# Kernel optimization log

Measured on AMD Instinct MI355X. Metric: run time of the kernel, lower is better.

Reference implementation:

```python
import jax, jax.numpy as jnp
import numpy as np

NA, NW, H = 20000, 100000, 128
DA, DW = 64, 128
E_CR, E_IN, E_CO = 400000, 600000, 300000


def _seg_softmax(logits, seg, n):
    m = jax.ops.segment_max(logits, seg, num_segments=n)
    e = jnp.exp(logits - m[seg])
    s = jax.ops.segment_sum(e, seg, num_segments=n)
    return e / (s[seg] + 1e-16)


def _gat(x_src, x_dst, edge, W, b, a_s, a_d):
    # PyG GATConv, heads=1, concat=False, shared lin for src/dst, add_self_loops=True
    n_src, n_dst = x_src.shape[0], x_dst.shape[0]
    loops = jnp.arange(min(n_src, n_dst), dtype=edge.dtype)
    src = jnp.concatenate([edge[0], loops])
    dst = jnp.concatenate([edge[1], loops])
    hs = x_src @ W            # [n_src, H]
    hd = x_dst @ W            # [n_dst, H]
    logit = jax.nn.leaky_relu((hs @ a_s)[src] + (hd @ a_d)[dst], 0.2)
    alpha = _seg_softmax(logit, dst, n_dst)          # softmax over in-neighborhoods
    out = jax.ops.segment_sum(alpha[:, None] * hs[src], dst, num_segments=n_dst)
    return out + b


def _mlp2(x, w1, b1, w2, b2):
    return jax.nn.relu(x @ w1 + b1) @ w2 + b2


def setup_inputs() -> dict:
    key = jax.random.key(0)
    ks = iter(jax.random.split(key, 40))

    def p(shape, scale=0.1):
        return jax.random.normal(next(ks), shape, jnp.float32) * scale

    def edges(n_src, n_dst, E):
        s = jax.random.randint(next(ks), (E,), 0, n_src, dtype=jnp.int32)
        d = jax.random.randint(next(ks), (E,), 0, n_dst, dtype=jnp.int32)
        d = jnp.where(s == d, (d + 1) % n_dst, d)  # keep input loop-free (PyG strips them)
        return jnp.stack([s, d])

    e_creates = edges(NA, NW, E_CR)
    inp = {
        'artist_feat': jax.random.normal(next(ks), (NA, DA), jnp.float32),
        'work_feat': jax.random.normal(next(ks), (NW, DW), jnp.float32),
        'a_w1': p((DA, H)), 'a_b1': jnp.zeros(H, jnp.float32),
        'a_w2': p((H, H)), 'a_b2': jnp.zeros(H, jnp.float32),
        'w_w1': p((DW, H)), 'w_b1': jnp.zeros(H, jnp.float32),
        'w_w2': p((H, H)), 'w_b2': jnp.zeros(H, jnp.float32),
        'cr_W': p((H, H)), 'cr_b': jnp.zeros(H, jnp.float32), 'cr_as': p((H,)), 'cr_ad': p((H,)),
        'in_W': p((H, H)), 'in_b': jnp.zeros(H, jnp.float32), 'in_as': p((H,)), 'in_ad': p((H,)),
        'co_W': p((H, H)), 'co_b': jnp.zeros(H, jnp.float32), 'co_as': p((H,)), 'co_ad': p((H,)),
        'p_w1': p((2 * H, 256)), 'p_b1': jnp.zeros(256, jnp.float32),
        'p_w2': p((256, 128)), 'p_b2': jnp.zeros(128, jnp.float32),
        'p_w3': p((128, 1)), 'p_b3': jnp.zeros(1, jnp.float32),
        'e_creates': e_creates,
        'e_created_by': jnp.flip(e_creates, axis=0),  # reverse relation [work, artist]
        'e_infl': edges(NW, NW, E_IN),
        'e_collab': edges(NA, NA, E_CO),
    }
    return inp


def reference(artist_feat, work_feat,
              a_w1, a_b1, a_w2, a_b2,
              w_w1, w_b1, w_w2, w_b2,
              cr_W, cr_b, cr_as, cr_ad,
              in_W, in_b, in_as, in_ad,
              co_W, co_b, co_as, co_ad,
              p_w1, p_b1, p_w2, p_b2, p_w3, p_b3,
              e_creates, e_created_by, e_infl, e_collab):
    ax = _mlp2(artist_feat, a_w1, a_b1, a_w2, a_b2)      # [NA, H]
    wx = _mlp2(work_feat, w_w1, w_b1, w_w2, w_b2)        # [NW, H]
    wx = jax.nn.elu(_gat(ax, wx, e_creates, cr_W, cr_b, cr_as, cr_ad))
    wx = jax.nn.elu(_gat(wx, wx, e_infl, in_W, in_b, in_as, in_ad))
    au = _gat(wx, ax, e_created_by, cr_W, cr_b, cr_as, cr_ad)  # no elu (matches source)
    ac = jax.nn.elu(_gat(au, au, e_collab, co_W, co_b, co_as, co_ad))
    comb = jnp.concatenate([au, ac], axis=1)             # [NA, 2H]
    h = jax.nn.relu(comb @ p_w1 + p_b1)                  # dropout is identity in eval
    h = jax.nn.relu(h @ p_w2 + p_b2)
    return (h @ p_w3 + p_b3).squeeze()
```

## Files before the change

### kernel.cpp

```cpp
#include <hip/hip_runtime.h>
#include <hip/hip_bf16.h>
#include <cstddef>

#define NA 20000
#define NW 100000
#define HH 128
#define DA 64
#define E_CR 400000
#define E_IN 600000
#define E_CO 300000

#define ROW1 0
#define ROW2 (NW)
#define ROW3 (2 * NW)
#define ROW4 (2 * NW + NA)
#define NTOT (2 * NW + 2 * NA)
#define CAPW 40
#define CAPA 88
#define NPREP (10 * 128 + 1)
#define GNB ((NA + 127) / 128)

typedef short v8s __attribute__((ext_vector_type(8)));
typedef float v4f __attribute__((ext_vector_type(4)));

constexpr int PSLOT = 2 * 128 * 264;

__device__ inline short f2bf(float x) {
    union { float f; unsigned u; } c; c.f = x;
    unsigned r = c.u + 0x7fff + ((c.u >> 16) & 1);
    return (short)(r >> 16);
}
__device__ inline float bf2f(short s) {
    union { unsigned u; float f; } c; c.u = ((unsigned)(unsigned short)s) << 16;
    return c.f;
}
__device__ inline float bfu2f(unsigned short s) {
    union { unsigned u; float f; } c; c.u = ((unsigned)s) << 16;
    return c.f;
}

__device__ inline void split8(const float* xv, v8s& h, v8s& l) {
#pragma unroll
    for (int p = 0; p < 4; ++p) {
        float2 xf; xf.x = xv[2 * p]; xf.y = xv[2 * p + 1];
        __hip_bfloat162 hb = __float22bfloat162_rn(xf);
        float2 hf = __bfloat1622float2(hb);
        float2 lf; lf.x = xf.x - hf.x; lf.y = xf.y - hf.y;
        __hip_bfloat162 lb = __float22bfloat162_rn(lf);
        union { __hip_bfloat162 b; short2 s; } uh, ul;
        uh.b = hb; ul.b = lb;
        h[2 * p] = uh.s.x; h[2 * p + 1] = uh.s.y;
        l[2 * p] = ul.s.x; l[2 * p + 1] = ul.s.y;
    }
}

struct AppChunk { const int* e; int E; int* pad; int cap; int* deg; };

__device__ inline void do_append(const AppChunk& ap, int bid) {
    int b0 = bid * 1024 + threadIdx.x;
    int s[4], d[4]; bool ok[4];
#pragma unroll
    for (int u = 0; u < 4; ++u) {
        int i = b0 + u * 256;
        ok[u] = i < ap.E;
        s[u] = 0; d[u] = 0;
        if (ok[u]) { s[u] = ap.e[i]; d[u] = ap.e[ap.E + i]; }
    }
    int p[4];
#pragma unroll
    for (int u = 0; u < 4; ++u) if (ok[u]) p[u] = atomicAdd(&ap.deg[d[u]], 1);
#pragma unroll
    for (int u = 0; u < 4; ++u)
        if (ok[u] && p[u] < ap.cap)
            ap.pad[(size_t)d[u] * ap.cap + p[u]] = s[u];
}

struct PrepDesc { const float* src; int ldw; int K; };
struct PrepArgs {
    PrepDesc d[10]; const float* wvW; const float* wvA; float* vd;
    const float* gX; const float* gB; float* gY; int gM;
};

__global__ __launch_bounds__(256) void k_prep_append(PrepArgs a, short* __restrict__ out,
                                                    AppChunk ap)
{
    __shared__ short Bs2[2 * 128 * 72];
    if (blockIdx.x >= NPREP + GNB) { do_append(ap, blockIdx.x - NPREP - GNB); return; }
    if (blockIdx.x >= NPREP) {
        int bid = blockIdx.x - NPREP;
        const int tid = threadIdx.x;
        const int wave = tid >> 6, lane = tid & 63;
        const int l15 = lane & 15, quad = lane >> 4;
        const int wrow = bid * 128 + wave * 32;
        for (int e = tid; e < 64 * 128; e += 256) {
            int n = e & 127, k = e >> 7;
            float x = a.d[0].src[(size_t)k * 128 + n];
            short h = f2bf(x);
            short l = f2bf(x - bf2f(h));
            Bs2[n * 72 + k] = h;
            Bs2[128 * 72 + n * 72 + k] = l;
        }
        v8s ah[2][2], al[2][2];
#pragma unroll
        for (int rf = 0; rf < 2; ++rf) {
            int r = wrow + rf * 16 + l15; if (r >= a.gM) r = a.gM - 1;
            const float* xp = a.gX + (size_t)r * DA + quad * 8;
#pragma unroll
            for (int kf = 0; kf < 2; ++kf) {
                float xv[8];
                *(float4*)&xv[0] = *(const float4*)(xp + kf * 32);
                *(float4*)&xv[4] = *(const float4*)(xp + kf * 32 + 4);
                split8(xv, ah[rf][kf], al[rf][kf]);
            }
        }
        __syncthreads();
        v4f acc[2][8];
#pragma unroll
        for (int rf = 0; rf < 2; ++rf)
#pragma unroll
            for (int cf = 0; cf < 8; ++cf) acc[rf][cf] = (v4f){0.f, 0.f, 0.f, 0.f};
#pragma unroll
        for (int kf = 0; kf < 2; ++kf) {
#pragma unroll
            for (int cf = 0; cf < 8; ++cf) {
                int coff = (cf * 16 + l15) * 72 + kf * 32 + quad * 8;
                v8s bh = *(const v8s*)&Bs2[coff];
                v8s bl = *(const v8s*)&Bs2[128 * 72 + coff];
#pragma unroll
                for (int rf = 0; rf < 2; ++rf) {
                    acc[rf][cf] = __builtin_amdgcn_mfma_f32_16x16x32_bf16(al[rf][kf], bh, acc[rf][cf], 0, 0, 0);
                    acc[rf][cf] = __builtin_amdgcn_mfma_f32_16x16x32_bf16(ah[rf][kf], bl, acc[rf][cf], 0, 0, 0);
                    acc[rf][cf] = __builtin_amdgcn_mfma_f32_16x16x32_bf16(ah[rf][kf], bh, acc[rf][cf], 0, 0, 0);
                }
            }
        }
        float bv[8];
#pragma unroll
        for (int cf = 0; cf < 8; ++cf) bv[cf] = a.gB[cf * 16 + l15];
#pragma unroll
        for (int rf = 0; rf < 2; ++rf) {
#pragma unroll
            for (int reg = 0; reg < 4; ++reg) {
                int r = wrow + rf * 16 + quad * 4 + reg;
                if (r >= a.gM) continue;
                float* yp = a.gY + (size_t)r * HH;
#pragma unroll
                for (int cf = 0; cf < 8; ++cf) {
                    float o = acc[rf][cf][reg] + bv[cf];
                    yp[cf * 16 + l15] = o > 0.f ? o : 0.f;
                }
            }
        }
        return;
    }
    if (blockIdx.x == NPREP - 1) {
        __shared__ float sa[HH];
        int t = threadIdx.x;
        if (t < HH) sa[t] = a.wvA[t];
        __syncthreads();
        if (t < HH) {
            float s = 0.f;
            for (int jj = 0; jj < HH; ++jj) s += a.wvW[(size_t)t * HH + jj] * sa[jj];
            a.vd[t] = s;
        }
        return;
    }
    int m = blockIdx.x >> 7;
    int e = (blockIdx.x & 127) * 256 + threadIdx.x;
    PrepDesc dd = a.d[m];
    int K = dd.K;
    int KP = (K <= 128) ? K + 8 : K;
    if (e >= K * 128) return;
    int n = e & 127, k = e >> 7;
    float x = dd.src[(size_t)k * dd.ldw + n];
    short h = f2bf(x);
    short l = f2bf(x - bf2f(h));
    short* base = out + (size_t)m * PSLOT;
    base[n * KP + k] = h;
    base[128 * KP + n * KP + k] = l;
}

template<int K, int ACT, int NSS, int ST, int LDSB, int OBF, int DUAL, int XBF>
__global__ __launch_bounds__(256, 2) void k_mfma(
    const float* __restrict__ X, int ldx,
    const short* __restrict__ Wp,
    const float* __restrict__ bias,
    float* __restrict__ Y, int ldy, int M,
    const float* __restrict__ v1, float* __restrict__ ss1,
    const float* __restrict__ v2, float* __restrict__ ss2,
    const float* __restrict__ sb)
{
    constexpr int KF = K / 32;
    constexpr int KP = LDSB ? K + 8 : K;
    __shared__ short Bs[LDSB ? 2 * 128 * (K + 8) : 8];
    const int tid = threadIdx.x;
    const int wave = tid >> 6, lane = tid & 63;
    const int l15 = lane & 15, quad = lane >> 4;
    int bid = blockIdx.x;
    if (DUAL) {
        int g0 = gridDim.x >> 1;
        if (bid >= g0) { bid -= g0; Wp += PSLOT; bias += 128; Y += 128; }
    }
    const int wrow = bid * 128 + wave * 32;

    if (LDSB) {
        const float4* src = (const float4*)Wp;
        float4* dst = (float4*)Bs;
        constexpr int total = 2 * 128 * KP / 8;
        for (int i = tid; i < total; i += 256) dst[i] = src[i];
    }

    v4f acc[2][8];
#pragma unroll
    for (int rf = 0; rf < 2; ++rf)
#pragma unroll
        for (int cf = 0; cf < 8; ++cf) acc[rf][cf] = (v4f){0.f, 0.f, 0.f, 0.f};

    v8s ah[2][KF], al[2][KF];
#pragma unroll
    for (int rf = 0; rf < 2; ++rf) {
        int r = wrow + rf * 16 + l15; if (r >= M) r = M - 1;
        if (XBF) {
            const unsigned short* xp = (const unsigned short*)X + (size_t)r * ldx + quad * 8;
#pragma unroll
            for (int kf = 0; kf < KF; ++kf)
                ah[rf][kf] = *(const v8s*)(xp + kf * 32);
        } else {
            const float* xp = X + (size_t)r * ldx + quad * 8;
#pragma unroll
            for (int kf = 0; kf < KF; ++kf) {
                float xv[8];
                *(float4*)&xv[0] = *(const float4*)(xp + kf * 32);
                *(float4*)&xv[4] = *(const float4*)(xp + kf * 32 + 4);
                split8(xv, ah[rf][kf], al[rf][kf]);
            }
        }
    }
    if (LDSB) __syncthreads();
#pragma unroll
    for (int kf = 0; kf < KF; ++kf) {
#pragma unroll
        for (int cf = 0; cf < 8; ++cf) {
            const short* bp = LDSB ? &Bs[(cf * 16 + l15) * KP + kf * 32 + quad * 8]
                                   : Wp + (size_t)(cf * 16 + l15) * K + kf * 32 + quad * 8;
            v8s bh = *(const v8s*)bp;
            v8s bl = *(const v8s*)(bp + 128 * KP);
#pragma unroll
            for (int rf = 0; rf < 2; ++rf) {
                if (!XBF) acc[rf][cf] = __builtin_amdgcn_mfma_f32_16x16x32_bf16(al[rf][kf], bh, acc[rf][cf], 0, 0, 0);
                acc[rf][cf] = __builtin_amdgcn_mfma_f32_16x16x32_bf16(ah[rf][kf], bl, acc[rf][cf], 0, 0, 0);
                acc[rf][cf] = __builtin_amdgcn_mfma_f32_16x16x32_bf16(ah[rf][kf], bh, acc[rf][cf], 0, 0, 0);
            }
        }
    }

    float bv[8], v1c[8], v2c[8];
#pragma unroll
    for (int cf = 0; cf < 8; ++cf) {
        int col = cf * 16 + l15;
        bv[cf] = bias ? bias[col] : 0.f;
        if (NSS >= 1) v1c[cf] = v1[col];
        if (NSS >= 2) v2c[cf] = v2[col];
    }
    float sbv = (NSS >= 1 && sb) ? sb[0] : 0.f;

#pragma unroll
    for (int rf = 0; rf < 2; ++rf) {
#pragma unroll
        for (int reg = 0; reg < 4; ++reg) {
            int r = wrow + rf * 16 + quad * 4 + reg;
            if (r >= M) continue;
            float p1 = 0.f, p2 = 0.f;
#pragma unroll
            for (int cf = 0; cf < 8; ++cf) {
                float o = acc[rf][cf][reg] + bv[cf];
                if (ACT == 1) o = o > 0.f ? o : 0.f;
                if (NSS >= 1) p1 = fmaf(o, v1c[cf], p1);
                if (NSS >= 2) p2 = fmaf(o, v2c[cf], p2);
                if (ST) {
                    if (OBF) ((unsigned short*)Y)[(size_t)r * ldy + cf * 16 + l15] = (unsigned short)f2bf(o);
                    else     Y[(size_t)r * ldy + cf * 16 + l15] = o;
                }
            }
            if (NSS >= 1) {
#pragma unroll
                for (int w = 1; w < 16; w <<= 1) {
                    p1 += __shfl_xor(p1, w, 64);
                    if (NSS >= 2) p2 += __shfl_xor(p2, w, 64);
                }
                if (l15 == 0) {
                    ss1[r] = p1 + sbv;
                    if (NSS >= 2) ss2[r] = p2;
                }
            }
        }
    }
}

struct MfmaCfg {
    const float* X; int ldx;
    const short* Wp;
    const float* bias;
    float* Y; int ldy; int M;
    int act, nss, obf, xbf, st;
    const float* v1; float* ss1;
    const float* v2; float* ss2;
    int nblocks;
};

__global__ __launch_bounds__(256, 2) void k_mfma2(MfmaCfg c0, MfmaCfg c1, AppChunk ap)
{
    constexpr int KF = 4, KP = 136;
    __shared__ short Bs[2 * 128 * KP];
    int bid = blockIdx.x;
    if (bid >= c0.nblocks + c1.nblocks) { do_append(ap, bid - c0.nblocks - c1.nblocks); return; }
    const bool first = bid < c0.nblocks;
    const MfmaCfg& c = first ? c0 : c1;
    if (!first) bid -= c0.nblocks;
    const int tid = threadIdx.x;
    const int wave = tid >> 6, lane = tid & 63;
    const int l15 = lane & 15, quad = lane >> 4;
    const int wrow = bid * 128 + wave * 32;

    {
        const float4* src = (const float4*)c.Wp;
        float4* dst = (float4*)Bs;
        constexpr int total = 2 * 128 * KP / 8;
        for (int i = tid; i < total; i += 256) dst[i] = src[i];
    }

    v4f acc[2][8];
#pragma unroll
    for (int rf = 0; rf < 2; ++rf)
#pragma unroll
        for (int cf = 0; cf < 8; ++cf) acc[rf][cf] = (v4f){0.f, 0.f, 0.f, 0.f};

    v8s ah[2][KF], al[2][KF];
#pragma unroll
    for (int rf = 0; rf < 2; ++rf) {
        int r = wrow + rf * 16 + l15; if (r >= c.M) r = c.M - 1;
        if (c.xbf) {
            const unsigned short* xp = (const unsigned short*)c.X + (size_t)r * c.ldx + quad * 8;
#pragma unroll
            for (int kf = 0; kf < KF; ++kf) {
                ah[rf][kf] = *(const v8s*)(xp + kf * 32);
                al[rf][kf] = (v8s)(short)0;
            }
        } else {
            const float* xp = c.X + (size_t)r * c.ldx + quad * 8;
#pragma unroll
            for (int kf = 0; kf < KF; ++kf) {
                float xv[8];
                *(float4*)&xv[0] = *(const float4*)(xp + kf * 32);
                *(float4*)&xv[4] = *(const float4*)(xp + kf * 32 + 4);
                split8(xv, ah[rf][kf], al[rf][kf]);
            }
        }
    }
    __syncthreads();
#pragma unroll
    for (int kf = 0; kf < KF; ++kf) {
#pragma unroll
        for (int cf = 0; cf < 8; ++cf) {
            const short* bp = &Bs[(cf * 16 + l15) * KP + kf * 32 + quad * 8];
            v8s bh = *(const v8s*)bp;
            v8s bl = *(const v8s*)(bp + 128 * KP);
#pragma unroll
            for (int rf = 0; rf < 2; ++rf) {
                if (!c.xbf) acc[rf][cf] = __builtin_amdgcn_mfma_f32_16x16x32_bf16(al[rf][kf], bh, acc[rf][cf], 0, 0, 0);
                acc[rf][cf] = __builtin_amdgcn_mfma_f32_16x16x32_bf16(ah[rf][kf], bl, acc[rf][cf], 0, 0, 0);
                acc[rf][cf] = __builtin_amdgcn_mfma_f32_16x16x32_bf16(ah[rf][kf], bh, acc[rf][cf], 0, 0, 0);
            }
        }
    }

    float bv[8], v1c[8], v2c[8];
#pragma unroll
    for (int cf = 0; cf < 8; ++cf) {
        int col = cf * 16 + l15;
        bv[cf] = c.bias ? c.bias[col] : 0.f;
        v1c[cf] = (c.nss >= 1) ? c.v1[col] : 0.f;
        v2c[cf] = (c.nss >= 2) ? c.v2[col] : 0.f;
    }

#pragma unroll
    for (int rf = 0; rf < 2; ++rf) {
#pragma unroll
        for (int reg = 0; reg < 4; ++reg) {
            int r = wrow + rf * 16 + quad * 4 + reg;
            if (r >= c.M) continue;
            float p1 = 0.f, p2 = 0.f;
#pragma unroll
            for (int cf = 0; cf < 8; ++cf) {
                float o = acc[rf][cf][reg] + bv[cf];
                if (c.act) o = o > 0.f ? o : 0.f;
                p1 = fmaf(o, v1c[cf], p1);
                p2 = fmaf(o, v2c[cf], p2);
                if (c.st) {
                    if (c.obf) ((unsigned short*)c.Y)[(size_t)r * c.ldy + cf * 16 + l15] = (unsigned short)f2bf(o);
                    else       c.Y[(size_t)r * c.ldy + cf * 16 + l15] = o;
                }
            }
            if (c.nss >= 1) {
#pragma unroll
                for (int w = 1; w < 16; w <<= 1) {
                    p1 += __shfl_xor(p1, w, 64);
                    p2 += __shfl_xor(p2, w, 64);
                }
                if (l15 == 0) {
                    c.ss1[r] = p1;
                    if (c.nss >= 2) c.ss2[r] = p2;
                }
            }
        }
    }
}

template<int ELU, int U, int CAP, int OBF>
__global__ __launch_bounds__(256) void k_aggregate(
    const int* __restrict__ deg, const int* __restrict__ esp,
    const unsigned short* __restrict__ hs, const float* __restrict__ ss,
    const float* __restrict__ sd, const float* __restrict__ bias,
    void* __restrict__ out, int ldy, int n, int loopn)
{
    int lane = threadIdx.x & 63;
    int wv = threadIdx.x >> 6;
    int d = blockIdx.x * 4 + wv;
    if (d >= n) return;
    int half = lane >> 5;
    int col = (lane & 31) * 4;
    const int* row = esp + (size_t)d * CAP;
    int i1 = deg[d]; if (i1 > CAP) i1 = CAP;
    float sdv = sd[d];
    float den = 0.f;
    float ax = 0.f, ay = 0.f, az = 0.f, aw = 0.f;
    if (half == 0 && d < loopn) {
        ushort4 h = *(const ushort4*)(hs + (size_t)d * HH + col);
        float l = ss[d] + sdv;
        l = l < 0.f ? 0.2f * l : l;
        float e = __expf(l);
        den += e;
        ax = fmaf(e, bfu2f(h.x), ax);
        ay = fmaf(e, bfu2f(h.y), ay);
        az = fmaf(e, bfu2f(h.z), az);
        aw = fmaf(e, bfu2f(h.w), aw);
    }
    int i = 0;
    for (; i + 2 * U <= i1; i += 2 * U) {
        int s[U]; ushort4 h[U]; float sv[U];
#pragma unroll
        for (int u = 0; u < U; ++u) s[u] = row[i + 2 * u + half];
#pragma unroll
        for (int u = 0; u < U; ++u) h[u] = *(const ushort4*)(hs + (size_t)s[u] * HH + col);
#pragma unroll
        for (int u = 0; u < U; ++u) sv[u] = ss[s[u]];
#pragma unroll
        for (int u = 0; u < U; ++u) {
            float l = sv[u] + sdv;
            l = l < 0.f ? 0.2f * l : l;
            float e = __expf(l);
            den += e;
            ax = fmaf(e, bfu2f(h[u].x), ax);
            ay = fmaf(e, bfu2f(h[u].y), ay);
            az = fmaf(e, bfu2f(h[u].z), az);
            aw = fmaf(e, bfu2f(h[u].w), aw);
        }
    }
    if (i < i1) {
        int s[U]; ushort4 h[U]; float sv[U]; bool act[U];
#pragma unroll
        for (int u = 0; u < U; ++u) {
            int idx = i + 2 * u + half;
            act[u] = idx < i1;
            s[u] = row[act[u] ? idx : (i1 - 1)];
        }
#pragma unroll
        for (int u = 0; u < U; ++u) h[u] = *(const ushort4*)(hs + (size_t)s[u] * HH + col);
#pragma unroll
        for (int u = 0; u < U; ++u) sv[u] = ss[s[u]];
#pragma unroll
        for (int u = 0; u < U; ++u) {
            float l = sv[u] + sdv;
            l = l < 0.f ? 0.2f * l : l;
            float e = act[u] ? __expf(l) : 0.f;
            den += e;
            ax = fmaf(e, bfu2f(h[u].x), ax);
            ay = fmaf(e, bfu2f(h[u].y), ay);
            az = fmaf(e, bfu2f(h[u].z), az);
            aw = fmaf(e, bfu2f(h[u].w), aw);
        }
    }
    den += __shfl_xor(den, 32, 64);
    ax += __shfl_xor(ax, 32, 64);
    ay += __shfl_xor(ay, 32, 64);
    az += __shfl_xor(az, 32, 64);
    aw += __shfl_xor(aw, 32, 64);
    if (half == 0) {
        float4 b = *(const float4*)(bias + col);
        float inv = 1.f / (den + 1e-16f);
        float o0 = ax * inv + b.x;
        float o1 = ay * inv + b.y;
        float o2 = az * inv + b.z;
        float o3 = aw * inv + b.w;
        if (ELU) {
            o0 = o0 > 0.f ? o0 : expm1f(o0);
            o1 = o1 > 0.f ? o1 : expm1f(o1);
            o2 = o2 > 0.f ? o2 : expm1f(o2);
            o3 = o3 > 0.f ? o3 : expm1f(o3);
        }
        if (OBF) {
            ushort4 ob;
            ob.x = (unsigned short)f2bf(o0);
            ob.y = (unsigned short)f2bf(o1);
            ob.z = (unsigned short)f2bf(o2);
            ob.w = (unsigned short)f2bf(o3);
            *(ushort4*)((unsigned short*)out + (size_t)d * ldy + col) = ob;
        } else {
            *(float4*)((float*)out + (size_t)d * ldy + col) = make_float4(o0, o1, o2, o3);
        }
    }
}

extern "C" void kernel_launch(void* const* d_in, const int* in_sizes, int n_in,
                              void* d_out, int out_size, void* d_ws, size_t ws_size,
                              hipStream_t stream)
{
    const float* artist = (const float*)d_in[0];
    const float* workf  = (const float*)d_in[1];
    const float* a_w1 = (const float*)d_in[2];  const float* a_b1 = (const float*)d_in[3];
    const float* a_w2 = (const float*)d_in[4];  const float* a_b2 = (const float*)d_in[5];
    const float* w_w1 = (const float*)d_in[6];  const float* w_b1 = (const float*)d_in[7];
    const float* w_w2 = (const float*)d_in[8];  const float* w_b2 = (const float*)d_in[9];
    const float* cr_W = (const float*)d_in[10]; const float* cr_b = (const float*)d_in[11];
    const float* cr_as = (const float*)d_in[12]; const float* cr_ad = (const float*)d_in[13];
    const float* in_W = (const float*)d_in[14]; const float* in_b = (const float*)d_in[15];
    const float* in_as = (const float*)d_in[16]; const float* in_ad = (const float*)d_in[17];
    const float* co_W = (const float*)d_in[18]; const float* co_b = (const float*)d_in[19];
    const float* co_as = (const float*)d_in[20]; const float* co_ad = (const float*)d_in[21];
    const float* p_w1 = (const float*)d_in[22]; const float* p_b1 = (const float*)d_in[23];
    const float* p_w2 = (const float*)d_in[24]; const float* p_b2 = (const float*)d_in[25];
    const float* p_w3 = (const float*)d_in[26]; const float* p_b3 = (const float*)d_in[27];
    const int* e_cr = (const int*)d_in[28];
    const int* e_cb = (const int*)d_in[29];
    const int* e_in = (const int*)d_in[30];
    const int* e_co = (const int*)d_in[31];

    char* wsp = (char*)d_ws;
    size_t off = 0;
    auto alloc = [&](size_t bytes) -> void* {
        void* p = wsp + off;
        off += (bytes + 255) / 256 * 256;
        return p;
    };
    float* ax   = (float*)alloc((size_t)NA * HH * 4);
    float* hsA  = (float*)alloc((size_t)NA * HH * 4);
    unsigned short* hsw = (unsigned short*)alloc((size_t)NW * HH * 2);
    unsigned short* wxb = (unsigned short*)alloc((size_t)NW * HH * 2);
    unsigned short* hsb = (unsigned short*)alloc((size_t)NW * HH * 2);
    float* h1   = (float*)alloc((size_t)NA * 256 * 4);
    float* comb = (float*)alloc((size_t)NA * 256 * 4);
    float* ss1 = (float*)alloc((size_t)NA * 4);
    float* sd1 = (float*)alloc((size_t)NW * 4);
    float* ss2 = (float*)alloc((size_t)NW * 4);
    float* sd2 = (float*)alloc((size_t)NW * 4);
    float* ss3 = (float*)alloc((size_t)NW * 4);
    float* sd3 = (float*)alloc((size_t)NA * 4);
    float* ss4 = (float*)alloc((size_t)NA * 4);
    float* sd4 = (float*)alloc((size_t)NA * 4);
    float* vd  = (float*)alloc(HH * 4);
    int* deg   = (int*)alloc((size_t)NTOT * 4);
    int* pad1  = (int*)alloc((size_t)NW * CAPW * 4);
    int* pad2  = (int*)alloc((size_t)NW * CAPW * 4);
    int* pad3  = (int*)alloc((size_t)NA * CAPA * 4);
    int* pad4  = (int*)alloc((size_t)NA * CAPA * 4);
    short* preW = (short*)alloc((size_t)10 * PSLOT * 2);
    (void)ws_size; (void)in_sizes; (void)n_in; (void)out_size;

    auto pre = [&](int m) { return preW + (size_t)m * PSLOT; };
    auto gg = [](int M) { return (M + 127) / 128; };
    auto apb = [](int E) { return (E + 1023) / 1024; };
    const float* nf = nullptr;
    float* nfm = nullptr;

    PrepArgs pa;
    pa.d[0] = {a_w1, HH, DA};
    pa.d[1] = {a_w2, HH, HH};
    pa.d[2] = {w_w1, HH, HH};
    pa.d[3] = {w_w2, HH, HH};
    pa.d[4] = {cr_W, HH, HH};
    pa.d[5] = {in_W, HH, HH};
    pa.d[6] = {co_W, HH, HH};
    pa.d[7] = {p_w1, 256, 256};
    pa.d[8] = {p_w1 + 128, 256, 256};
    pa.d[9] = {p_w2, HH, 256};
    pa.wvW = cr_W; pa.wvA = cr_ad; pa.vd = vd;
    pa.gX = artist; pa.gB = a_b1; pa.gY = hsA; pa.gM = NA;

    AppChunk ap1 = {e_cr, E_CR, pad1, CAPW, deg + ROW1};
    AppChunk ap2 = {e_in, E_IN, pad2, CAPW, deg + ROW2};
    AppChunk ap3 = {e_cb, E_CR, pad3, CAPA, deg + ROW3};
    AppChunk ap4 = {e_co, E_CO, pad4, CAPA, deg + ROW4};

    (void)hipMemsetAsync(deg, 0, (size_t)NTOT * 4, stream);

    k_prep_append<<<NPREP + GNB + apb(E_CR), 256, 0, stream>>>(pa, preW, ap1);

    {
        MfmaCfg c0 = {workf, HH, pre(2), w_b1, (float*)hsw, HH, NW, 1, 0, 1, 0, 1, nf, nfm, nf, nfm, gg(NW)};
        MfmaCfg c1 = {hsA, HH, pre(1), a_b2, ax, HH, NA, 0, 1, 0, 0, 1, vd, sd3, nf, nfm, gg(NA)};
        k_mfma2<<<gg(NW) + gg(NA) + apb(E_IN), 256, 0, stream>>>(c0, c1, ap2);
    }
    {
        MfmaCfg c0 = {(const float*)hsw, HH, pre(3), w_b2, nfm, HH, NW, 0, 1, 0, 1, 0, vd, sd1, nf, nfm, gg(NW)};
        MfmaCfg c1 = {ax, HH, pre(4), nullptr, (float*)hsb, HH, NA, 0, 1, 1, 0, 1, cr_as, ss1, nf, nfm, gg(NA)};
        k_mfma2<<<gg(NW) + gg(NA) + apb(E_CR), 256, 0, stream>>>(c0, c1, ap3);
    }

    k_aggregate<1, 2, CAPW, 1><<<(NW + 3) / 4, 256, 0, stream>>>(deg + ROW1, pad1, hsb, ss1, sd1, cr_b, wxb, HH, NW, NA);

    {
        MfmaCfg c0 = {(const float*)wxb, HH, pre(5), nullptr, (float*)hsb, HH, NW, 0, 2, 1, 1, 1, in_as, ss2, in_ad, sd2, gg(NW)};
        MfmaCfg c1 = {nullptr, 0, nullptr, nullptr, nullptr, 0, 0, 0, 0, 0, 0, 0, nf, nfm, nf, nfm, 0};
        k_mfma2<<<gg(NW) + apb(E_CO), 256, 0, stream>>>(c0, c1, ap4);
    }
    k_aggregate<1, 2, CAPW, 1><<<(NW + 3) / 4, 256, 0, stream>>>(deg + ROW2, pad2, hsb, ss2, sd2, in_b, wxb, HH, NW, NW);

    k_mfma<HH, 0, 1, 1, 1, 1, 0, 1><<<gg(NW), 256, 0, stream>>>((const float*)wxb, HH, pre(4), nullptr, (float*)hsb, HH, NW, cr_as, ss3, nf, nfm, nf);
    k_aggregate<0, 4, CAPA, 0><<<(NA + 3) / 4, 256, 0, stream>>>(deg + ROW3, pad3, hsb, ss3, sd3, cr_b, comb, 256, NA, NA);

    k_mfma<HH, 0, 2, 1, 1, 1, 0, 0><<<gg(NA), 256, 0, stream>>>(comb, 256, pre(6), nullptr, (float*)hsb, HH, NA, co_as, ss4, co_ad, sd4, nf);
    k_aggregate<1, 4, CAPA, 0><<<(NA + 3) / 4, 256, 0, stream>>>(deg + ROW4, pad4, hsb, ss4, sd4, co_b, comb + 128, 256, NA, NA);

    k_mfma<256, 1, 0, 1, 0, 0, 1, 0><<<2 * gg(NA), 256, 0, stream>>>(comb, 256, pre(7), p_b1, h1, 256, NA, nf, nfm, nf, nfm, nf);
    k_mfma<256, 1, 1, 0, 0, 0, 0, 0><<<gg(NA), 256, 0, stream>>>(h1, 256, pre(9), p_b2, nfm, 0, NA, p_w3, (float*)d_out, nf, nfm, p_b3);
}
```

Before: 576.8 us.

## Fold work MLP second layer into destination attention score vector

```diff
diff --git a/kernel.cpp b/kernel.cpp
--- a/kernel.cpp
+++ b/kernel.cpp
@@ -79,6 +79,7 @@
 struct PrepArgs {
     PrepDesc d[10]; const float* wvW; const float* wvA; float* vd;
     const float* gX; const float* gB; float* gY; int gM;
+    const float* w2W; const float* w2B; float* ud; float* sb1;
 };
 
 __global__ __launch_bounds__(256) void k_prep_append(PrepArgs a, short* __restrict__ out,
@@ -155,13 +156,29 @@
     }
     if (blockIdx.x == NPREP - 1) {
         __shared__ float sa[HH];
+        __shared__ float sv[HH];
+        __shared__ float sp[HH];
         int t = threadIdx.x;
         if (t < HH) sa[t] = a.wvA[t];
         __syncthreads();
+        float vdt = 0.f;
+        if (t < HH) {
+            for (int jj = 0; jj < HH; ++jj) vdt += a.wvW[(size_t)t * HH + jj] * sa[jj];
+            a.vd[t] = vdt;
+            sv[t] = vdt;
+        }
+        __syncthreads();
         if (t < HH) {
             float s = 0.f;
-            for (int jj = 0; jj < HH; ++jj) s += a.wvW[(size_t)t * HH + jj] * sa[jj];
-            a.vd[t] = s;
+            for (int jj = 0; jj < HH; ++jj) s += a.w2W[(size_t)t * HH + jj] * sv[jj];
+            a.ud[t] = s;
+            sp[t] = a.w2B[t] * sv[t];
+        }
+        __syncthreads();
+        if (t == 0) {
+            float s = 0.f;
+            for (int jj = 0; jj < HH; ++jj) s += sp[jj];
+            a.sb1[0] = s;
         }
         return;
     }
@@ -305,6 +322,7 @@
     int act, nss, obf, xbf, st;
     const float* v1; float* ss1;
     const float* v2; float* ss2;
+    const float* sb;
     int nblocks;
 };
 
@@ -382,6 +400,7 @@
         v1c[cf] = (c.nss >= 1) ? c.v1[col] : 0.f;
         v2c[cf] = (c.nss >= 2) ? c.v2[col] : 0.f;
     }
+    float sbv = (c.nss >= 1 && c.sb) ? c.sb[0] : 0.f;
 
 #pragma unroll
     for (int rf = 0; rf < 2; ++rf) {
@@ -408,7 +427,7 @@
                     p2 += __shfl_xor(p2, w, 64);
                 }
                 if (l15 == 0) {
-                    c.ss1[r] = p1;
+                    c.ss1[r] = p1 + sbv;
                     if (c.nss >= 2) c.ss2[r] = p2;
                 }
             }
@@ -568,6 +587,8 @@
     float* ss4 = (float*)alloc((size_t)NA * 4);
     float* sd4 = (float*)alloc((size_t)NA * 4);
     float* vd  = (float*)alloc(HH * 4);
+    float* ud  = (float*)alloc(HH * 4);
+    float* sb1 = (float*)alloc(4);
     int* deg   = (int*)alloc((size_t)NTOT * 4);
     int* pad1  = (int*)alloc((size_t)NW * CAPW * 4);
     int* pad2  = (int*)alloc((size_t)NW * CAPW * 4);
@@ -595,6 +616,7 @@
     pa.d[9] = {p_w2, HH, 256};
     pa.wvW = cr_W; pa.wvA = cr_ad; pa.vd = vd;
     pa.gX = artist; pa.gB = a_b1; pa.gY = hsA; pa.gM = NA;
+    pa.w2W = w_w2; pa.w2B = w_b2; pa.ud = ud; pa.sb1 = sb1;
 
     AppChunk ap1 = {e_cr, E_CR, pad1, CAPW, deg + ROW1};
     AppChunk ap2 = {e_in, E_IN, pad2, CAPW, deg + ROW2};
@@ -606,21 +628,21 @@
     k_prep_append<<<NPREP + GNB + apb(E_CR), 256, 0, stream>>>(pa, preW, ap1);
 
     {
-        MfmaCfg c0 = {workf, HH, pre(2), w_b1, (float*)hsw, HH, NW, 1, 0, 1, 0, 1, nf, nfm, nf, nfm, gg(NW)};
-        MfmaCfg c1 = {hsA, HH, pre(1), a_b2, ax, HH, NA, 0, 1, 0, 0, 1, vd, sd3, nf, nfm, gg(NA)};
+        MfmaCfg c0 = {workf, HH, pre(2), w_b1, (float*)hsw, HH, NW, 1, 1, 1, 0, 1, ud, sd1, nf, nfm, sb1, gg(NW)};
+        MfmaCfg c1 = {hsA, HH, pre(1), a_b2, ax, HH, NA, 0, 1, 0, 0, 1, vd, sd3, nf, nfm, nf, gg(NA)};
         k_mfma2<<<gg(NW) + gg(NA) + apb(E_IN), 256, 0, stream>>>(c0, c1, ap2);
     }
     {
-        MfmaCfg c0 = {(const float*)hsw, HH, pre(3), w_b2, nfm, HH, NW, 0, 1, 0, 1, 0, vd, sd1, nf, nfm, gg(NW)};
-        MfmaCfg c1 = {ax, HH, pre(4), nullptr, (float*)hsb, HH, NA, 0, 1, 1, 0, 1, cr_as, ss1, nf, nfm, gg(NA)};
-        k_mfma2<<<gg(NW) + gg(NA) + apb(E_CR), 256, 0, stream>>>(c0, c1, ap3);
+        MfmaCfg c0 = {ax, HH, pre(4), nullptr, (float*)hsb, HH, NA, 0, 1, 1, 0, 1, cr_as, ss1, nf, nfm, nf, gg(NA)};
+        MfmaCfg c1 = {nullptr, 0, nullptr, nullptr, nullptr, 0, 0, 0, 0, 0, 0, 0, nf, nfm, nf, nfm, nf, 0};
+        k_mfma2<<<gg(NA) + apb(E_CR), 256, 0, stream>>>(c0, c1, ap3);
     }
 
     k_aggregate<1, 2, CAPW, 1><<<(NW + 3) / 4, 256, 0, stream>>>(deg + ROW1, pad1, hsb, ss1, sd1, cr_b, wxb, HH, NW, NA);
 
     {
-        MfmaCfg c0 = {(const float*)wxb, HH, pre(5), nullptr, (float*)hsb, HH, NW, 0, 2, 1, 1, 1, in_as, ss2, in_ad, sd2, gg(NW)};
-        MfmaCfg c1 = {nullptr, 0, nullptr, nullptr, nullptr, 0, 0, 0, 0, 0, 0, 0, nf, nfm, nf, nfm, 0};
+        MfmaCfg c0 = {(const float*)wxb, HH, pre(5), nullptr, (float*)hsb, HH, NW, 0, 2, 1, 1, 1, in_as, ss2, in_ad, sd2, nf, gg(NW)};
+        MfmaCfg c1 = {nullptr, 0, nullptr, nullptr, nullptr, 0, 0, 0, 0, 0, 0, 0, nf, nfm, nf, nfm, nf, 0};
         k_mfma2<<<gg(NW) + apb(E_CO), 256, 0, stream>>>(c0, c1, ap4);
     }
     k_aggregate<1, 2, CAPW, 1><<<(NW + 3) / 4, 256, 0, stream>>>(deg + ROW2, pad2, hsb, ss2, sd2, in_b, wxb, HH, NW, NW);
```

Result: no change. 580.4 us (+0.6%).
